# Performance work log

Hardware: AMD Instinct MI355X
Metric: run time of the kernel (lower is better)

Reference implementation:

```python
import jax, jax.numpy as jnp
import numpy as np

BS, N, H, F_IN, F_OUT = 4, 2048, 2, 768, 768
NEG_SLOPE = 0.2

def setup_inputs() -> dict:
    key = jax.random.key(0)
    k_h, k_adj, k_w, k_as, k_ad = jax.random.split(key, 5)
    h = jax.random.normal(k_h, (BS, N, F_IN), dtype=jnp.float32)
    adj = jax.random.randint(k_adj, (BS, N, N), 0, 2) > 0  # bool adjacency
    # xavier_uniform fan_in/fan_out per torch semantics on [H, f_in, f_out]
    limit_w = float(np.sqrt(6.0 / (F_IN + F_OUT)))
    w = jax.random.uniform(k_w, (H, F_IN, F_OUT), minval=-limit_w, maxval=limit_w, dtype=jnp.float32)
    limit_a = float(np.sqrt(6.0 / (F_OUT + 1)))
    a_src = jax.random.uniform(k_as, (H, F_OUT, 1), minval=-limit_a, maxval=limit_a, dtype=jnp.float32)
    a_dst = jax.random.uniform(k_ad, (H, F_OUT, 1), minval=-limit_a, maxval=limit_a, dtype=jnp.float32)
    bias = jnp.zeros((F_OUT,), dtype=jnp.float32)
    return {"h": h, "adj": adj, "w": w, "a_src": a_src, "a_dst": a_dst, "bias": bias}

def reference(h, adj, w, a_src, a_dst, bias):
    # h: [b, n, f_in]; w: [H, f_in, f_out] -> h_prime: [b, H, n, f_out]
    h_prime = jnp.einsum('bnf,hfo->bhno', h, w)
    t = jnp.tanh(h_prime)
    attn_src = jnp.einsum('bhno,ho->bhn', t, a_src[..., 0])  # [b, H, n]
    attn_dst = jnp.einsum('bhno,ho->bhn', t, a_dst[..., 0])  # [b, H, n]
    # broadcast add: scores[b,h,i,j] = src[i] + dst[j]
    attn = attn_src[:, :, :, None] + attn_dst[:, :, None, :]
    attn = jnp.where(attn >= 0, attn, NEG_SLOPE * attn)  # leaky_relu
    n = adj.shape[-1]
    keep = adj[:, None, :, :] | jnp.eye(n, dtype=bool)[None, None]  # [b,1,n,n]
    attn = jnp.where(keep, attn, -jnp.inf)
    attn = jax.nn.softmax(attn, axis=-1)
    # dropout is identity at inference
    out = jnp.einsum('bhij,bhjo->bhio', attn, h_prime)
    return out + bias
```

## Files before the change

kernel.cpp:

```cpp
#include <hip/hip_runtime.h>
#include <hip/hip_bf16.h>
#include <cstdint>
#include <cstddef>

#define BS   4
#define NN   2048
#define NH   2
#define FIN  768
#define FOUT 768
#define NEG_SLOPE 0.2f

typedef __attribute__((ext_vector_type(8))) short short8;
typedef __attribute__((ext_vector_type(4))) float float4v;

static __device__ __forceinline__ float bits2f(unsigned short u) {
    union { unsigned int i; float f; } v; v.i = ((unsigned int)u) << 16; return v.f;
}
static __device__ __forceinline__ unsigned short f2bits(float f) {
    union { float f; unsigned int i; } v; v.f = f;
    unsigned int x = v.i;
    unsigned int r = x + 0x7fffu + ((x >> 16) & 1u);
    return (unsigned short)(r >> 16);
}
static __device__ __forceinline__ float fast_tanh(float x) {
    float xc = fminf(fmaxf(x, -20.f), 20.f);
    float e = __expf(2.f * xc);
    return (e - 1.f) / (e + 1.f);
}
static __device__ __forceinline__ void async_copy16(void* lds, const void* g) {
    __builtin_amdgcn_global_load_lds(
        (const __attribute__((address_space(1))) unsigned int*)g,
        (__attribute__((address_space(3))) unsigned int*)lds, 16, 0, 0);
}

static __device__ __forceinline__ bool detect_isf32(const unsigned short* h_raw) {
    unsigned short u = h_raw[threadIdx.x & 63];
    int e = (u >> 7) & 0xFF;
    unsigned long long m = __ballot(e >= 118 && e <= 134);
    return __popcll(m) < 48;
}
static __device__ __forceinline__ bool detect_adj8(const unsigned char* adj_raw) {
    int l = threadIdx.x & 63;
    unsigned char v = (unsigned char)(adj_raw[l * 4 + 1] | adj_raw[l * 4 + 2] |
                                      adj_raw[l * 4 + 3]);
    unsigned long long m = __ballot(v != 0);
    return __popcll(m) > 8;
}

__global__ __launch_bounds__(256) void k_misc(
    float* __restrict__ attn_acc,
    const void* __restrict__ as_raw, const void* __restrict__ ad_raw,
    const void* __restrict__ b_raw, const unsigned short* __restrict__ h_raw,
    float* __restrict__ asf, float* __restrict__ adf, float* __restrict__ bff)
{
    const int nzb = (2 * BS * NH * NN) / 256;
    int bi = blockIdx.x;
    if (bi < nzb) {
        attn_acc[bi * 256 + threadIdx.x] = 0.f;
        return;
    }
    bool isf = detect_isf32(h_raw);
    int t = threadIdx.x;
    for (int i = t; i < NH * FOUT; i += 256) {
        asf[i] = isf ? ((const float*)as_raw)[i] : bits2f(((const unsigned short*)as_raw)[i]);
        adf[i] = isf ? ((const float*)ad_raw)[i] : bits2f(((const unsigned short*)ad_raw)[i]);
    }
    for (int i = t; i < FOUT; i += 256)
        bff[i] = isf ? ((const float*)b_raw)[i] : bits2f(((const unsigned short*)b_raw)[i]);
}

__global__ __launch_bounds__(256) void k_prep_h(
    const void* __restrict__ hr, unsigned short* __restrict__ dst, int n)
{
    bool isf = detect_isf32((const unsigned short*)hr);
    int base = (blockIdx.x * 256 + threadIdx.x) * 8;
    if (base >= n) return;
    if (isf) {
        float4 f0 = *((const float4*)((const float*)hr + base));
        float4 f1 = *((const float4*)((const float*)hr + base + 4));
        unsigned short v[8] = { f2bits(f0.x), f2bits(f0.y), f2bits(f0.z), f2bits(f0.w),
                                f2bits(f1.x), f2bits(f1.y), f2bits(f1.z), f2bits(f1.w) };
        *(uint4*)(dst + base) = *(const uint4*)v;
    } else {
        *(uint4*)(dst + base) = *(const uint4*)((const unsigned short*)hr + base);
    }
}

__global__ __launch_bounds__(256) void k_prep_w(
    const void* __restrict__ wr, unsigned short* __restrict__ wth,
    const unsigned short* __restrict__ h_raw)
{
    bool isf = detect_isf32(h_raw);
    __shared__ float tile[32][33];
    int h  = blockIdx.z;
    int f0 = blockIdx.x * 32;
    int o0 = blockIdx.y * 32;
    int tx = threadIdx.x, ty = threadIdx.y;
    #pragma unroll
    for (int r = 0; r < 4; ++r) {
        int fl = ty * 4 + r;
        size_t idx = (size_t)h * FIN * FOUT + (size_t)(f0 + fl) * FOUT + (o0 + tx);
        tile[fl][tx] = isf ? ((const float*)wr)[idx]
                           : bits2f(((const unsigned short*)wr)[idx]);
    }
    __syncthreads();
    #pragma unroll
    for (int r = 0; r < 4; ++r) {
        int ol = ty * 4 + r;
        size_t oidx = (size_t)h * FOUT * FIN + (size_t)(o0 + ol) * FIN + (f0 + tx);
        wth[oidx] = f2bits(tile[tx][ol]);
    }
}

#define BM 128
#define BN 128
#define BK 32

__global__ __launch_bounds__(256) void k_gemm_hw(
    const unsigned short* __restrict__ hh,
    const unsigned short* __restrict__ wh,
    unsigned short* __restrict__ hpT,
    const float* __restrict__ asf, const float* __restrict__ adf,
    float* __restrict__ attn_src, float* __restrict__ attn_dst)
{
    int ib = blockIdx.z;
    int b  = ib / NH, hd = ib % NH;
    int i0 = blockIdx.x * BM;
    int o0 = blockIdx.y * BN;
    const unsigned short* A  = hh + (size_t)b  * NN * FIN;
    const unsigned short* Bt = wh + (size_t)hd * FOUT * FIN;
    unsigned short*       C  = hpT + (size_t)ib * FOUT * NN;

    __shared__ __align__(16) unsigned short As[BM * BK];
    __shared__ __align__(16) unsigned short Bs[BN * BK];

    int t = threadIdx.x;
    int lane = t & 63, wave = t >> 6;
    int wm = (wave & 1) * 64, wn = (wave >> 1) * 64;
    int lm = lane & 15, quad = lane >> 4;
    int rr = lane >> 2;
    int cc = (lane & 3) ^ ((rr >> 1) & 3);
    int sA = (lm >> 1) & 3;

    float4v acc[4][4] = {};

    for (int k0 = 0; k0 < FIN; k0 += BK) {
        __syncthreads();
        #pragma unroll
        for (int p = 0; p < 2; ++p) {
            int r0 = wave * 32 + p * 16;
            async_copy16(&As[r0 * BK], A  + (size_t)(i0 + r0 + rr) * FIN + k0 + cc * 8);
            async_copy16(&Bs[r0 * BK], Bt + (size_t)(o0 + r0 + rr) * FIN + k0 + cc * 8);
        }
        __syncthreads();
        short8 fa[4], fb[4];
        #pragma unroll
        for (int mt = 0; mt < 4; ++mt)
            fa[mt] = *(const short8*)&As[(wm + mt * 16 + lm) * BK + ((quad ^ sA) * 8)];
        #pragma unroll
        for (int nt = 0; nt < 4; ++nt)
            fb[nt] = *(const short8*)&Bs[(wn + nt * 16 + lm) * BK + ((quad ^ sA) * 8)];
        #pragma unroll
        for (int mt = 0; mt < 4; ++mt)
            #pragma unroll
            for (int nt = 0; nt < 4; ++nt)
                acc[mt][nt] = __builtin_amdgcn_mfma_f32_16x16x32_bf16(
                    fa[mt], fb[nt], acc[mt][nt], 0, 0, 0);
    }

    float asv[4], adv[4];
    #pragma unroll
    for (int nt = 0; nt < 4; ++nt) {
        int o = o0 + wn + nt * 16 + lm;
        asv[nt] = asf[hd * FOUT + o];
        adv[nt] = adf[hd * FOUT + o];
    }
    #pragma unroll
    for (int mt = 0; mt < 4; ++mt) {
        float ps[4] = {0.f, 0.f, 0.f, 0.f};
        float pd[4] = {0.f, 0.f, 0.f, 0.f};
        #pragma unroll
        for (int nt = 0; nt < 4; ++nt) {
            int node = i0 + wm + mt * 16 + quad * 4;
            int o    = o0 + wn + nt * 16 + lm;
            ushort4 v;
            v.x = f2bits(acc[mt][nt][0]);
            v.y = f2bits(acc[mt][nt][1]);
            v.z = f2bits(acc[mt][nt][2]);
            v.w = f2bits(acc[mt][nt][3]);
            *(ushort4*)&C[(size_t)o * NN + node] = v;
            #pragma unroll
            for (int r = 0; r < 4; ++r) {
                float tv = fast_tanh(acc[mt][nt][r]);
                ps[r] += tv * asv[nt];
                pd[r] += tv * adv[nt];
            }
        }
        #pragma unroll
        for (int r = 0; r < 4; ++r) {
            float s = ps[r], d = pd[r];
            #pragma unroll
            for (int off = 1; off <= 8; off <<= 1) {
                s += __shfl_xor(s, off);
                d += __shfl_xor(d, off);
            }
            if (lm == 0) {
                int node = i0 + wm + mt * 16 + quad * 4 + r;
                atomicAdd(&attn_src[ib * NN + node], s);
                atomicAdd(&attn_dst[ib * NN + node], d);
            }
        }
    }
}

__global__ __launch_bounds__(256) void k_softmax_p(
    const float* __restrict__ attn_src, const float* __restrict__ attn_dst,
    const void* __restrict__ adj_raw,
    unsigned short* __restrict__ P)
{
    int blk = blockIdx.x;
    int i = blk & (NN - 1);
    int b = blk >> 11;
    bool is8 = detect_adj8((const unsigned char*)adj_raw);
    int t = threadIdx.x;
    int lane = t & 63, wave = t >> 6;
    int j0 = t * 8;

    bool keep[8];
    if (is8) {
        const unsigned char* arow = (const unsigned char*)adj_raw + ((size_t)b * NN + i) * NN;
        uint2 v = *(const uint2*)(arow + j0);
        #pragma unroll
        for (int r = 0; r < 8; ++r) {
            unsigned int w = (r < 4) ? v.x : v.y;
            keep[r] = ((w >> ((r & 3) * 8)) & 0xFFu) != 0;
        }
    } else {
        const int* arow = (const int*)adj_raw + ((size_t)b * NN + i) * NN;
        int4 v0 = *(const int4*)(arow + j0);
        int4 v1 = *(const int4*)(arow + j0 + 4);
        keep[0] = v0.x != 0; keep[1] = v0.y != 0; keep[2] = v0.z != 0; keep[3] = v0.w != 0;
        keep[4] = v1.x != 0; keep[5] = v1.y != 0; keep[6] = v1.z != 0; keep[7] = v1.w != 0;
    }
    #pragma unroll
    for (int r = 0; r < 8; ++r) keep[r] = keep[r] || (j0 + r == i);

    __shared__ float redm[4], reds[4];
    for (int hh = 0; hh < NH; ++hh) {
        int bh = b * NH + hh;
        float src = attn_src[bh * NN + i];
        const float* drow = attn_dst + (size_t)bh * NN;
        float4 d0 = *(const float4*)(drow + j0);
        float4 d1 = *(const float4*)(drow + j0 + 4);
        float dj[8] = { d0.x, d0.y, d0.z, d0.w, d1.x, d1.y, d1.z, d1.w };

        float s[8];
        float lmax = -1e30f;
        #pragma unroll
        for (int r = 0; r < 8; ++r) {
            float sc = src + dj[r];
            sc = sc >= 0.f ? sc : NEG_SLOPE * sc;
            s[r] = keep[r] ? sc : -1e30f;
            lmax = fmaxf(lmax, s[r]);
        }
        __syncthreads();
        #pragma unroll
        for (int off = 32; off > 0; off >>= 1)
            lmax = fmaxf(lmax, __shfl_xor(lmax, off));
        if (lane == 0) redm[wave] = lmax;
        __syncthreads();
        float m = fmaxf(fmaxf(redm[0], redm[1]), fmaxf(redm[2], redm[3]));

        float p[8];
        float lsum = 0.f;
        #pragma unroll
        for (int r = 0; r < 8; ++r) {
            p[r] = __expf(s[r] - m);
            lsum += p[r];
        }
        #pragma unroll
        for (int off = 32; off > 0; off >>= 1)
            lsum += __shfl_xor(lsum, off);
        if (lane == 0) reds[wave] = lsum;
        __syncthreads();
        float inv = 1.0f / (reds[0] + reds[1] + reds[2] + reds[3]);

        uint4 pw;
        pw.x = ((unsigned int)f2bits(p[1] * inv) << 16) | f2bits(p[0] * inv);
        pw.y = ((unsigned int)f2bits(p[3] * inv) << 16) | f2bits(p[2] * inv);
        pw.z = ((unsigned int)f2bits(p[5] * inv) << 16) | f2bits(p[4] * inv);
        pw.w = ((unsigned int)f2bits(p[7] * inv) << 16) | f2bits(p[6] * inv);
        *(uint4*)&P[((size_t)bh * NN + i) * NN + j0] = pw;
    }
}

__global__ __launch_bounds__(256) void k_gemm_out(
    const unsigned short* __restrict__ P,
    const unsigned short* __restrict__ hpT,
    const float* __restrict__ bf,
    void* __restrict__ outp, const unsigned short* __restrict__ h_raw)
{
    bool isf = detect_isf32(h_raw);
    int ib = blockIdx.z;
    int i0 = blockIdx.x * BM;
    int o0 = blockIdx.y * BN;
    const unsigned short* A  = P   + (size_t)ib * NN * NN;
    const unsigned short* Bt = hpT + (size_t)ib * FOUT * NN;

    __shared__ __align__(16) unsigned short As[BM * BK];
    __shared__ __align__(16) unsigned short Bs[BN * BK];

    int t = threadIdx.x;
    int lane = t & 63, wave = t >> 6;
    int wm = (wave & 1) * 64, wn = (wave >> 1) * 64;
    int lm = lane & 15, quad = lane >> 4;
    int rr = lane >> 2;
    int cc = (lane & 3) ^ ((rr >> 1) & 3);
    int sA = (lm >> 1) & 3;

    float4v acc[4][4] = {};

    for (int k0 = 0; k0 < NN; k0 += BK) {
        __syncthreads();
        #pragma unroll
        for (int p = 0; p < 2; ++p) {
            int r0 = wave * 32 + p * 16;
            async_copy16(&As[r0 * BK], A  + (size_t)(i0 + r0 + rr) * NN + k0 + cc * 8);
            async_copy16(&Bs[r0 * BK], Bt + (size_t)(o0 + r0 + rr) * NN + k0 + cc * 8);
        }
        __syncthreads();
        short8 fa[4], fb[4];
        #pragma unroll
        for (int mt = 0; mt < 4; ++mt)
            fa[mt] = *(const short8*)&As[(wm + mt * 16 + lm) * BK + ((quad ^ sA) * 8)];
        #pragma unroll
        for (int nt = 0; nt < 4; ++nt)
            fb[nt] = *(const short8*)&Bs[(wn + nt * 16 + lm) * BK + ((quad ^ sA) * 8)];
        #pragma unroll
        for (int mt = 0; mt < 4; ++mt)
            #pragma unroll
            for (int nt = 0; nt < 4; ++nt)
                acc[mt][nt] = __builtin_amdgcn_mfma_f32_16x16x32_bf16(
                    fa[mt], fb[nt], acc[mt][nt], 0, 0, 0);
    }

    if (isf) {
        float* C = (float*)outp + (size_t)ib * NN * FOUT;
        #pragma unroll
        for (int nt = 0; nt < 4; ++nt) {
            int o = o0 + wn + nt * 16 + lm;
            float bv = bf[o];
            #pragma unroll
            for (int mt = 0; mt < 4; ++mt) {
                int i = i0 + wm + mt * 16 + quad * 4;
                #pragma unroll
                for (int r = 0; r < 4; ++r)
                    C[(size_t)(i + r) * FOUT + o] = acc[mt][nt][r] + bv;
            }
        }
    } else {
        unsigned short* C = (unsigned short*)outp + (size_t)ib * NN * FOUT;
        #pragma unroll
        for (int nt = 0; nt < 4; ++nt) {
            int o = o0 + wn + nt * 16 + lm;
            float bv = bf[o];
            #pragma unroll
            for (int mt = 0; mt < 4; ++mt) {
                int i = i0 + wm + mt * 16 + quad * 4;
                #pragma unroll
                for (int r = 0; r < 4; ++r)
                    C[(size_t)(i + r) * FOUT + o] = f2bits(acc[mt][nt][r] + bv);
            }
        }
    }
}

extern "C" void kernel_launch(void* const* d_in, const int* in_sizes, int n_in,
                              void* d_out, int out_size, void* d_ws, size_t ws_size,
                              hipStream_t stream)
{
    const void* h_raw   = d_in[0];
    const void* adj_raw = d_in[1];
    const void* w_raw   = d_in[2];
    const void* as_raw  = d_in[3];
    const void* ad_raw  = d_in[4];
    const void* b_raw   = d_in[5];

    char* ws = (char*)d_ws;
    size_t off = 0;
    unsigned short* hpT = (unsigned short*)(ws + off); off += (size_t)BS * NH * FOUT * NN * 2;
    float* asr = (float*)(ws + off);            off += (size_t)BS * NH * NN * 4;
    float* ads = (float*)(ws + off);            off += (size_t)BS * NH * NN * 4;
    size_t uoff = off;
    unsigned short* P    = (unsigned short*)(ws + uoff);
    unsigned short* h_bf = (unsigned short*)(ws + uoff); uoff += (size_t)BS * NN * FIN * 2;
    unsigned short* wt_b = (unsigned short*)(ws + uoff); uoff += (size_t)NH * FOUT * FIN * 2;
    off += (size_t)BS * NH * NN * NN * 2;
    float* asf = (float*)(ws + off);            off += (size_t)NH * FOUT * 4;
    float* adf = (float*)(ws + off);            off += (size_t)NH * FOUT * 4;
    float* bff = (float*)(ws + off);            off += 4096;

    int n_h = BS * NN * FIN;

    k_misc<<<(2 * BS * NH * NN) / 256 + 1, 256, 0, stream>>>(
        asr, as_raw, ad_raw, b_raw, (const unsigned short*)h_raw, asf, adf, bff);
    k_prep_h<<<n_h / (256 * 8), 256, 0, stream>>>(h_raw, h_bf, n_h);
    k_prep_w<<<dim3(FIN / 32, FOUT / 32, NH), dim3(32, 8), 0, stream>>>(
        w_raw, wt_b, (const unsigned short*)h_raw);
    k_gemm_hw<<<dim3(NN / BM, FOUT / BN, BS * NH), 256, 0, stream>>>(
        h_bf, wt_b, hpT, asf, adf, asr, ads);
    k_softmax_p<<<dim3(BS * NN), 256, 0, stream>>>(asr, ads, adj_raw, P);
    k_gemm_out<<<dim3(NN / BM, FOUT / BN, BS * NH), 256, 0, stream>>>(
        P, hpT, bff, d_out, (const unsigned short*)h_raw);
}
```

Measured before the change: 296.9 us.

## Merge prep kernels, double GEMM K-tile with new swizzle, reorder output grid

Folds the h conversion, W transpose, accumulator zeroing and parameter conversion into one launch, removing two kernel launches. Both GEMMs now stage 64-wide K tiles with a reworked XOR swizzle and run two MFMA sub-steps per barrier pair, halving the number of synchronisations. The output GEMM grid is swapped so consecutive blocks walk the output-feature dimension, keeping a P row-tile hot in cache. The cost is doubled LDS per block, which may lower occupancy, and a more intricate swizzle that has to stay bank-conflict free.

```diff
diff --git a/kernel.cpp b/kernel.cpp
--- a/kernel.cpp
+++ b/kernel.cpp
@@ -47,20 +47,63 @@
     return __popcll(m) > 8;
 }
 
-__global__ __launch_bounds__(256) void k_misc(
-    float* __restrict__ attn_acc,
+#define NB_H   3072
+#define NB_W   1152
+#define NB_Z   128
+__global__ __launch_bounds__(256) void k_prep(
+    const void* __restrict__ hr, unsigned short* __restrict__ h_bf,
+    const void* __restrict__ wr, unsigned short* __restrict__ wt_b,
     const void* __restrict__ as_raw, const void* __restrict__ ad_raw,
-    const void* __restrict__ b_raw, const unsigned short* __restrict__ h_raw,
-    float* __restrict__ asf, float* __restrict__ adf, float* __restrict__ bff)
+    const void* __restrict__ b_raw,
+    float* __restrict__ asf, float* __restrict__ adf, float* __restrict__ bff,
+    float* __restrict__ attn_acc)
 {
-    const int nzb = (2 * BS * NH * NN) / 256;
+    __shared__ float tile[32][33];
     int bi = blockIdx.x;
-    if (bi < nzb) {
-        attn_acc[bi * 256 + threadIdx.x] = 0.f;
+    int t = threadIdx.x;
+    if (bi < NB_H) {
+        bool isf = detect_isf32((const unsigned short*)hr);
+        int base = (bi * 256 + t) * 8;
+        if (isf) {
+            float4 f0 = *((const float4*)((const float*)hr + base));
+            float4 f1 = *((const float4*)((const float*)hr + base + 4));
+            unsigned short v[8] = { f2bits(f0.x), f2bits(f0.y), f2bits(f0.z), f2bits(f0.w),
+                                    f2bits(f1.x), f2bits(f1.y), f2bits(f1.z), f2bits(f1.w) };
+            *(uint4*)(h_bf + base) = *(const uint4*)v;
+        } else {
+            *(uint4*)(h_bf + base) = *(const uint4*)((const unsigned short*)hr + base);
+        }
         return;
     }
-    bool isf = detect_isf32(h_raw);
-    int t = threadIdx.x;
+    if (bi < NB_H + NB_W) {
+        bool isf = detect_isf32((const unsigned short*)hr);
+        int wb = bi - NB_H;
+        int h  = wb / 576;
+        int rem = wb % 576;
+        int f0 = (rem % 24) * 32;
+        int o0 = (rem / 24) * 32;
+        int tx = t & 31, ty = t >> 5;
+        #pragma unroll
+        for (int r = 0; r < 4; ++r) {
+            int fl = ty * 4 + r;
+            size_t idx = (size_t)h * FIN * FOUT + (size_t)(f0 + fl) * FOUT + (o0 + tx);
+            tile[fl][tx] = isf ? ((const float*)wr)[idx]
+                               : bits2f(((const unsigned short*)wr)[idx]);
+        }
+        __syncthreads();
+        #pragma unroll
+        for (int r = 0; r < 4; ++r) {
+            int ol = ty * 4 + r;
+            size_t oidx = (size_t)h * FOUT * FIN + (size_t)(o0 + ol) * FIN + (f0 + tx);
+            wt_b[oidx] = f2bits(tile[tx][ol]);
+        }
+        return;
+    }
+    if (bi < NB_H + NB_W + NB_Z) {
+        attn_acc[(bi - NB_H - NB_W) * 256 + t] = 0.f;
+        return;
+    }
+    bool isf = detect_isf32((const unsigned short*)hr);
     for (int i = t; i < NH * FOUT; i += 256) {
         asf[i] = isf ? ((const float*)as_raw)[i] : bits2f(((const unsigned short*)as_raw)[i]);
         adf[i] = isf ? ((const float*)ad_raw)[i] : bits2f(((const unsigned short*)ad_raw)[i]);
@@ -69,52 +112,9 @@
         bff[i] = isf ? ((const float*)b_raw)[i] : bits2f(((const unsigned short*)b_raw)[i]);
 }
 
-__global__ __launch_bounds__(256) void k_prep_h(
-    const void* __restrict__ hr, unsigned short* __restrict__ dst, int n)
-{
-    bool isf = detect_isf32((const unsigned short*)hr);
-    int base = (blockIdx.x * 256 + threadIdx.x) * 8;
-    if (base >= n) return;
-    if (isf) {
-        float4 f0 = *((const float4*)((const float*)hr + base));
-        float4 f1 = *((const float4*)((const float*)hr + base + 4));
-        unsigned short v[8] = { f2bits(f0.x), f2bits(f0.y), f2bits(f0.z), f2bits(f0.w),
-                                f2bits(f1.x), f2bits(f1.y), f2bits(f1.z), f2bits(f1.w) };
-        *(uint4*)(dst + base) = *(const uint4*)v;
-    } else {
-        *(uint4*)(dst + base) = *(const uint4*)((const unsigned short*)hr + base);
-    }
-}
-
-__global__ __launch_bounds__(256) void k_prep_w(
-    const void* __restrict__ wr, unsigned short* __restrict__ wth,
-    const unsigned short* __restrict__ h_raw)
-{
-    bool isf = detect_isf32(h_raw);
-    __shared__ float tile[32][33];
-    int h  = blockIdx.z;
-    int f0 = blockIdx.x * 32;
-    int o0 = blockIdx.y * 32;
-    int tx = threadIdx.x, ty = threadIdx.y;
-    #pragma unroll
-    for (int r = 0; r < 4; ++r) {
-        int fl = ty * 4 + r;
-        size_t idx = (size_t)h * FIN * FOUT + (size_t)(f0 + fl) * FOUT + (o0 + tx);
-        tile[fl][tx] = isf ? ((const float*)wr)[idx]
-                           : bits2f(((const unsigned short*)wr)[idx]);
-    }
-    __syncthreads();
-    #pragma unroll
-    for (int r = 0; r < 4; ++r) {
-        int ol = ty * 4 + r;
-        size_t oidx = (size_t)h * FOUT * FIN + (size_t)(o0 + ol) * FIN + (f0 + tx);
-        wth[oidx] = f2bits(tile[tx][ol]);
-    }
-}
-
 #define BM 128
 #define BN 128
-#define BK 32
+#define BK 64
 
 __global__ __launch_bounds__(256) void k_gemm_hw(
     const unsigned short* __restrict__ hh,
@@ -138,34 +138,40 @@
     int lane = t & 63, wave = t >> 6;
     int wm = (wave & 1) * 64, wn = (wave >> 1) * 64;
     int lm = lane & 15, quad = lane >> 4;
-    int rr = lane >> 2;
-    int cc = (lane & 3) ^ ((rr >> 1) & 3);
+    int rr = lane >> 3;
+    int cc = lane & 7;
+    int gc = ((cc & 3) ^ ((rr >> 1) & 3)) | ((((cc >> 2) ^ rr) & 1) << 2);
     int sA = (lm >> 1) & 3;
+    int sP = lm & 1;
 
     float4v acc[4][4] = {};
 
     for (int k0 = 0; k0 < FIN; k0 += BK) {
         __syncthreads();
         #pragma unroll
-        for (int p = 0; p < 2; ++p) {
-            int r0 = wave * 32 + p * 16;
-            async_copy16(&As[r0 * BK], A  + (size_t)(i0 + r0 + rr) * FIN + k0 + cc * 8);
-            async_copy16(&Bs[r0 * BK], Bt + (size_t)(o0 + r0 + rr) * FIN + k0 + cc * 8);
-        }
-        __syncthreads();
-        short8 fa[4], fb[4];
-        #pragma unroll
-        for (int mt = 0; mt < 4; ++mt)
-            fa[mt] = *(const short8*)&As[(wm + mt * 16 + lm) * BK + ((quad ^ sA) * 8)];
-        #pragma unroll
-        for (int nt = 0; nt < 4; ++nt)
-            fb[nt] = *(const short8*)&Bs[(wn + nt * 16 + lm) * BK + ((quad ^ sA) * 8)];
-        #pragma unroll
-        for (int mt = 0; mt < 4; ++mt)
+        for (int p = 0; p < 4; ++p) {
+            int r0 = wave * 32 + p * 8;
+            async_copy16(&As[r0 * BK], A  + (size_t)(i0 + r0 + rr) * FIN + k0 + gc * 8);
+            async_copy16(&Bs[r0 * BK], Bt + (size_t)(o0 + r0 + rr) * FIN + k0 + gc * 8);
+        }
+        __syncthreads();
+        #pragma unroll
+        for (int kk = 0; kk < 2; ++kk) {
+            int so = ((kk ^ sP) << 2);
+            short8 fa[4], fb[4];
+            #pragma unroll
+            for (int mt = 0; mt < 4; ++mt)
+                fa[mt] = *(const short8*)&As[(wm + mt * 16 + lm) * BK + (so + (quad ^ sA)) * 8];
             #pragma unroll
             for (int nt = 0; nt < 4; ++nt)
-                acc[mt][nt] = __builtin_amdgcn_mfma_f32_16x16x32_bf16(
-                    fa[mt], fb[nt], acc[mt][nt], 0, 0, 0);
+                fb[nt] = *(const short8*)&Bs[(wn + nt * 16 + lm) * BK + (so + (quad ^ sA)) * 8];
+            #pragma unroll
+            for (int mt = 0; mt < 4; ++mt)
+                #pragma unroll
+                for (int nt = 0; nt < 4; ++nt)
+                    acc[mt][nt] = __builtin_amdgcn_mfma_f32_16x16x32_bf16(
+                        fa[mt], fb[nt], acc[mt][nt], 0, 0, 0);
+        }
     }
 
     float asv[4], adv[4];
@@ -302,8 +308,8 @@
 {
     bool isf = detect_isf32(h_raw);
     int ib = blockIdx.z;
-    int i0 = blockIdx.x * BM;
-    int o0 = blockIdx.y * BN;
+    int o0 = blockIdx.x * BN;
+    int i0 = blockIdx.y * BM;
     const unsigned short* A  = P   + (size_t)ib * NN * NN;
     const unsigned short* Bt = hpT + (size_t)ib * FOUT * NN;
 
@@ -314,34 +320,40 @@
     int lane = t & 63, wave = t >> 6;
     int wm = (wave & 1) * 64, wn = (wave >> 1) * 64;
     int lm = lane & 15, quad = lane >> 4;
-    int rr = lane >> 2;
-    int cc = (lane & 3) ^ ((rr >> 1) & 3);
+    int rr = lane >> 3;
+    int cc = lane & 7;
+    int gc = ((cc & 3) ^ ((rr >> 1) & 3)) | ((((cc >> 2) ^ rr) & 1) << 2);
     int sA = (lm >> 1) & 3;
+    int sP = lm & 1;
 
     float4v acc[4][4] = {};
 
     for (int k0 = 0; k0 < NN; k0 += BK) {
         __syncthreads();
         #pragma unroll
-        for (int p = 0; p < 2; ++p) {
-            int r0 = wave * 32 + p * 16;
-            async_copy16(&As[r0 * BK], A  + (size_t)(i0 + r0 + rr) * NN + k0 + cc * 8);
-            async_copy16(&Bs[r0 * BK], Bt + (size_t)(o0 + r0 + rr) * NN + k0 + cc * 8);
-        }
-        __syncthreads();
-        short8 fa[4], fb[4];
-        #pragma unroll
-        for (int mt = 0; mt < 4; ++mt)
-            fa[mt] = *(const short8*)&As[(wm + mt * 16 + lm) * BK + ((quad ^ sA) * 8)];
-        #pragma unroll
-        for (int nt = 0; nt < 4; ++nt)
-            fb[nt] = *(const short8*)&Bs[(wn + nt * 16 + lm) * BK + ((quad ^ sA) * 8)];
-        #pragma unroll
-        for (int mt = 0; mt < 4; ++mt)
+        for (int p = 0; p < 4; ++p) {
+            int r0 = wave * 32 + p * 8;
+            async_copy16(&As[r0 * BK], A  + (size_t)(i0 + r0 + rr) * NN + k0 + gc * 8);
+            async_copy16(&Bs[r0 * BK], Bt + (size_t)(o0 + r0 + rr) * NN + k0 + gc * 8);
+        }
+        __syncthreads();
+        #pragma unroll
+        for (int kk = 0; kk < 2; ++kk) {
+            int so = ((kk ^ sP) << 2);
+            short8 fa[4], fb[4];
+            #pragma unroll
+            for (int mt = 0; mt < 4; ++mt)
+                fa[mt] = *(const short8*)&As[(wm + mt * 16 + lm) * BK + (so + (quad ^ sA)) * 8];
             #pragma unroll
             for (int nt = 0; nt < 4; ++nt)
-                acc[mt][nt] = __builtin_amdgcn_mfma_f32_16x16x32_bf16(
-                    fa[mt], fb[nt], acc[mt][nt], 0, 0, 0);
+                fb[nt] = *(const short8*)&Bs[(wn + nt * 16 + lm) * BK + (so + (quad ^ sA)) * 8];
+            #pragma unroll
+            for (int mt = 0; mt < 4; ++mt)
+                #pragma unroll
+                for (int nt = 0; nt < 4; ++nt)
+                    acc[mt][nt] = __builtin_amdgcn_mfma_f32_16x16x32_bf16(
+                        fa[mt], fb[nt], acc[mt][nt], 0, 0, 0);
+        }
     }
 
     if (isf) {
@@ -400,16 +412,11 @@
     float* adf = (float*)(ws + off);            off += (size_t)NH * FOUT * 4;
     float* bff = (float*)(ws + off);            off += 4096;
 
-    int n_h = BS * NN * FIN;
-
-    k_misc<<<(2 * BS * NH * NN) / 256 + 1, 256, 0, stream>>>(
-        asr, as_raw, ad_raw, b_raw, (const unsigned short*)h_raw, asf, adf, bff);
-    k_prep_h<<<n_h / (256 * 8), 256, 0, stream>>>(h_raw, h_bf, n_h);
-    k_prep_w<<<dim3(FIN / 32, FOUT / 32, NH), dim3(32, 8), 0, stream>>>(
-        w_raw, wt_b, (const unsigned short*)h_raw);
+    k_prep<<<NB_H + NB_W + NB_Z + 1, 256, 0, stream>>>(
+        h_raw, h_bf, w_raw, wt_b, as_raw, ad_raw, b_raw, asf, adf, bff, asr);
     k_gemm_hw<<<dim3(NN / BM, FOUT / BN, BS * NH), 256, 0, stream>>>(
         h_bf, wt_b, hpT, asf, adf, asr, ads);
     k_softmax_p<<<dim3(BS * NN), 256, 0, stream>>>(asr, ads, adj_raw, P);
-    k_gemm_out<<<dim3(NN / BM, FOUT / BN, BS * NH), 256, 0, stream>>>(
+    k_gemm_out<<<dim3(FOUT / BN, NN / BM, BS * NH), 256, 0, stream>>>(
         P, hpT, bff, d_out, (const unsigned short*)h_raw);
 }
```

New measurement: 297.4 us. No clear change (+0.1%).
